# Kernel optimization log

Measured on AMD Instinct MI355X. Metric: run time of the kernel, lower is better.

The kernel has to match this reference:

```python
import jax, jax.numpy as jnp
import numpy as np


def _wasserstein_1d(xs, a, b, p):
    # POT-style 1D OT loss on shared sorted support xs: sum over merged
    # quantile levels of |F_a^{-1}(q) - F_b^{-1}(q)|^p * dq  (no p-th root).
    n = xs.shape[0]
    cdf_a = jnp.cumsum(a)
    cdf_b = jnp.cumsum(b)
    qs = jnp.sort(jnp.concatenate([cdf_a, cdf_b]))  # [2n] merged quantile levels
    qa = xs[jnp.clip(jnp.searchsorted(cdf_a, qs), 0, n - 1)]
    qb = xs[jnp.clip(jnp.searchsorted(cdf_b, qs), 0, n - 1)]
    qs_pad = jnp.concatenate([jnp.zeros((1,), qs.dtype), qs])
    delta = qs_pad[1:] - qs_pad[:-1]
    return jnp.sum(delta * jnp.abs(qa - qb) ** p)


def setup_inputs() -> dict:
    key = jax.random.key(0)
    k1, k2 = jax.random.split(key)
    N = 8388608      # samples
    NBINS = 10       # discretization
    G = 4            # number of groups
    acts = jax.random.normal(k1, (N,), dtype=jnp.float32)
    group_labels = jax.random.randint(k2, (N,), 0, G, dtype=jnp.int32)
    bary_est = jnp.ones((NBINS,), jnp.float32) / NBINS  # learned barycenter param, init 1/n
    return {"acts": acts, "bary_est": bary_est, "group_labels": group_labels,
            "nbins": NBINS, "n_groups": G}


def reference(acts, bary_est, group_labels, nbins, n_groups):
    r = 1.0 / nbins
    locs = jnp.arange(0, 1, r, dtype=acts.dtype)              # [nbins] bin centers
    c = jax.nn.sigmoid(acts) - 0.0001                         # [N] cdf-mapped samples
    # triangular-kernel soft histogram contributions: [N, nbins]
    K = jax.nn.relu(r - jnp.abs(c[:, None] - locs[None, :]))
    # per-group bin counts (torch.unique returns sorted labels 0..G-1)
    counts = jax.ops.segment_sum(K, group_labels, num_segments=n_groups)  # [G, nbins]
    h = counts + 0.0001
    h = h / jnp.sum(h, axis=1, keepdims=True)   # HistoBin norm
    h = h / jnp.sum(h, axis=1, keepdims=True)   # genHists renorm (mathematical no-op, kept for fidelity)
    xs = jnp.arange(nbins, dtype=acts.dtype)    # POT support bins 0..n-1
    losses = jax.vmap(lambda hg: _wasserstein_1d(xs, hg, bary_est, 2))(h)  # [G]
    loss = jnp.sum(losses).reshape(1)
    return loss, bary_est
```

## Files before the change

kernel.cpp:

```cpp
#include <hip/hip_runtime.h>

#define NBINS 10
#define NG 4
#define NH (NG * NBINS)
#define TPB 128
#define NBLOCKS 2048
#define PACKF 32.0f

__device__ __forceinline__ void proc1(float x, int g, float* col) {
    float ex = __expf(-x);
    float rc = __builtin_amdgcn_rcpf(1.0f + ex);
    float p  = __builtin_fmaf(rc, 10.0f, -0.001f);
    float fj = floorf(p);
    float u  = p - fj;
    int j0 = max((int)fj, 0);
    int row = g * NBINS + j0;
    col[row * TPB] += (PACKF + u);
}

__device__ __forceinline__ void proc4(float4 a, int4 g, float* col) {
    proc1(a.x, g.x, col); proc1(a.y, g.y, col);
    proc1(a.z, g.z, col); proc1(a.w, g.w, col);
}

__global__ void __launch_bounds__(TPB) wb_hist(const float4* __restrict__ acts,
                                               const int4* __restrict__ labels,
                                               const float* __restrict__ acts_s,
                                               const int* __restrict__ labels_s,
                                               float* __restrict__ parts,
                                               int n4, int n, int nparts) {
    __shared__ float lh[NH * TPB];
    const int tid = threadIdx.x;
    #pragma unroll
    for (int i = 0; i < NH; ++i) lh[i * TPB + tid] = 0.0f;
    __syncthreads();

    float* col = &lh[tid];
    const int gsz = gridDim.x * TPB;
    int idx = blockIdx.x * TPB + tid;
    for (; idx + 3 * gsz < n4; idx += 4 * gsz) {
        float4 a0 = acts[idx];
        float4 a1 = acts[idx + gsz];
        float4 a2 = acts[idx + 2 * gsz];
        float4 a3 = acts[idx + 3 * gsz];
        int4 g0 = labels[idx];
        int4 g1 = labels[idx + gsz];
        int4 g2 = labels[idx + 2 * gsz];
        int4 g3 = labels[idx + 3 * gsz];
        proc4(a0, g0, col); proc4(a1, g1, col);
        proc4(a2, g2, col); proc4(a3, g3, col);
    }
    for (; idx < n4; idx += gsz) proc4(acts[idx], labels[idx], col);

    if (blockIdx.x == 0 && tid == 0) {
        for (int i = n4 * 4; i < n; ++i) proc1(acts_s[i], labels_s[i], col);
    }
    __syncthreads();

    if (tid < NH) {
        float n_sum = 0.0f, u_sum = 0.0f;
        for (int k = 0; k < TPB; ++k) {
            float acc = lh[tid * TPB + ((tid + k) & (TPB - 1))];
            float nc = floorf(acc * (1.0f / PACKF));
            n_sum += nc;
            u_sum += acc - PACKF * nc;
        }
        float u_prev = __shfl_up(u_sum, 1);
        if ((tid % NBINS) == 0) u_prev = 0.0f;
        parts[tid * nparts + blockIdx.x] = 0.1f * (n_sum - u_sum + u_prev);
    }
}

__global__ void __launch_bounds__(1024) wb_final(const float4* __restrict__ parts4,
                                                 const float* __restrict__ bary,
                                                 float* __restrict__ out, int nparts) {
    __shared__ float hist[NH];
    __shared__ float bsh[NBINS];
    __shared__ float losses[NG];

    if (threadIdx.x < NBINS) {
        float b = bary[threadIdx.x];
        bsh[threadIdx.x] = b;
        out[1 + threadIdx.x] = b;
    }

    const int q4 = nparts >> 2;
    int wave = threadIdx.x >> 6, lane = threadIdx.x & 63;
    for (int j = wave; j < NH; j += 16) {
        float s = 0.0f;
        for (int i = lane; i < q4; i += 64) {
            float4 v = parts4[j * q4 + i];
            s += (v.x + v.y) + (v.z + v.w);
        }
        #pragma unroll
        for (int off = 32; off; off >>= 1) s += __shfl_down(s, off);
        if (lane == 0) hist[j] = s;
    }
    __syncthreads();

    if (threadIdx.x < NG) {
        const int gI = threadIdx.x;
        float h[NBINS];
        float s = 0.0f;
        #pragma unroll
        for (int j = 0; j < NBINS; ++j) { h[j] = hist[gI * NBINS + j] + 0.0001f; s += h[j]; }
        #pragma unroll
        for (int j = 0; j < NBINS; ++j) h[j] /= s;
        float s2 = 0.0f;
        #pragma unroll
        for (int j = 0; j < NBINS; ++j) s2 += h[j];
        #pragma unroll
        for (int j = 0; j < NBINS; ++j) h[j] /= s2;

        float cdfa[NBINS], cdfb[NBINS];
        float acc = 0.0f;
        #pragma unroll
        for (int j = 0; j < NBINS; ++j) { acc += h[j]; cdfa[j] = acc; }
        acc = 0.0f;
        #pragma unroll
        for (int j = 0; j < NBINS; ++j) { acc += bsh[j]; cdfb[j] = acc; }
        float T = fmaxf(cdfa[NBINS - 1], cdfb[NBINS - 1]);
        cdfa[NBINS - 1] = T;
        cdfb[NBINS - 1] = T;

        float loss = 0.0f, lo_a = 0.0f;
        #pragma unroll
        for (int i = 0; i < NBINS; ++i) {
            float hi_a = cdfa[i];
            float lo_b = 0.0f;
            #pragma unroll
            for (int j = 0; j < NBINS; ++j) {
                float hi_b = cdfb[j];
                float ov = fminf(hi_a, hi_b) - fmaxf(lo_a, lo_b);
                float w = (float)((i - j) * (i - j));
                loss += fmaxf(ov, 0.0f) * w;
                lo_b = hi_b;
            }
            lo_a = hi_a;
        }
        losses[gI] = loss;
    }
    __syncthreads();
    if (threadIdx.x == 0)
        out[0] = losses[0] + losses[1] + losses[2] + losses[3];
}

extern "C" void kernel_launch(void* const* d_in, const int* in_sizes, int n_in,
                              void* d_out, int out_size, void* d_ws, size_t ws_size,
                              hipStream_t stream) {
    const float* acts   = (const float*)d_in[0];
    const float* bary   = (const float*)d_in[1];
    const int*   labels = (const int*)d_in[2];
    float* outp  = (float*)d_out;
    float* parts = (float*)d_ws;
    int N  = in_sizes[0];
    int n4 = N >> 2;

    wb_hist<<<NBLOCKS, TPB, 0, stream>>>((const float4*)acts, (const int4*)labels,
                                         acts, labels, parts, n4, N, NBLOCKS);
    wb_final<<<1, 1024, 0, stream>>>((const float4*)parts, bary, outp, NBLOCKS);
}
```

Baseline: 31.56 us.

## Fuse histogram and final loss kernels with last-block ticket reduction

```diff
diff --git a/kernel.cpp b/kernel.cpp
--- a/kernel.cpp
+++ b/kernel.cpp
@@ -23,13 +23,20 @@
     proc1(a.z, g.z, col); proc1(a.w, g.w, col);
 }
 
-__global__ void __launch_bounds__(TPB) wb_hist(const float4* __restrict__ acts,
-                                               const int4* __restrict__ labels,
-                                               const float* __restrict__ acts_s,
-                                               const int* __restrict__ labels_s,
-                                               float* __restrict__ parts,
-                                               int n4, int n, int nparts) {
+__global__ void __launch_bounds__(TPB) wb_fused(const float4* __restrict__ acts,
+                                                const int4* __restrict__ labels,
+                                                const float* __restrict__ acts_s,
+                                                const int* __restrict__ labels_s,
+                                                const float* __restrict__ bary,
+                                                float* __restrict__ out,
+                                                float* __restrict__ parts,
+                                                unsigned int* __restrict__ ticket,
+                                                int n4, int n) {
     __shared__ float lh[NH * TPB];
+    float* hist   = &lh[0];
+    float* losses = &lh[48];
+    volatile unsigned int* lastflag = (volatile unsigned int*)&lh[56];
+
     const int tid = threadIdx.x;
     #pragma unroll
     for (int i = 0; i < NH; ++i) lh[i * TPB + tid] = 0.0f;
@@ -67,39 +74,39 @@
         }
         float u_prev = __shfl_up(u_sum, 1);
         if ((tid % NBINS) == 0) u_prev = 0.0f;
-        parts[tid * nparts + blockIdx.x] = 0.1f * (n_sum - u_sum + u_prev);
-    }
-}
-
-__global__ void __launch_bounds__(1024) wb_final(const float4* __restrict__ parts4,
-                                                 const float* __restrict__ bary,
-                                                 float* __restrict__ out, int nparts) {
-    __shared__ float hist[NH];
-    __shared__ float bsh[NBINS];
-    __shared__ float losses[NG];
-
-    if (threadIdx.x < NBINS) {
-        float b = bary[threadIdx.x];
-        bsh[threadIdx.x] = b;
-        out[1 + threadIdx.x] = b;
-    }
-
-    const int q4 = nparts >> 2;
-    int wave = threadIdx.x >> 6, lane = threadIdx.x & 63;
-    for (int j = wave; j < NH; j += 16) {
-        float s = 0.0f;
-        for (int i = lane; i < q4; i += 64) {
-            float4 v = parts4[j * q4 + i];
-            s += (v.x + v.y) + (v.z + v.w);
-        }
-        #pragma unroll
-        for (int off = 32; off; off >>= 1) s += __shfl_down(s, off);
-        if (lane == 0) hist[j] = s;
+        float hb = 0.1f * (n_sum - u_sum + u_prev);
+        __hip_atomic_store(&parts[tid * NBLOCKS + blockIdx.x], hb,
+                           __ATOMIC_RELAXED, __HIP_MEMORY_SCOPE_AGENT);
     }
     __syncthreads();
 
-    if (threadIdx.x < NG) {
-        const int gI = threadIdx.x;
+    if (tid == 0) {
+        unsigned int old = __hip_atomic_fetch_add(ticket, 1u, __ATOMIC_RELAXED,
+                                                  __HIP_MEMORY_SCOPE_AGENT);
+        *lastflag = (old == (unsigned int)(NBLOCKS - 1)) ? 1u : 0u;
+    }
+    __syncthreads();
+    if (*lastflag == 0u) return;
+
+    {
+        int wave = tid >> 6, lane = tid & 63;
+        for (int j = wave; j < NH; j += 2) {
+            float s = 0.0f;
+            #pragma unroll
+            for (int k = 0; k < NBLOCKS / 64; ++k)
+                s += __hip_atomic_load(&parts[j * NBLOCKS + lane + k * 64],
+                                       __ATOMIC_RELAXED, __HIP_MEMORY_SCOPE_AGENT);
+            #pragma unroll
+            for (int off = 32; off; off >>= 1) s += __shfl_down(s, off);
+            if (lane == 0) hist[j] = s;
+        }
+    }
+    if (tid >= NH && tid < NH + NBINS)
+        out[1 + (tid - NH)] = bary[tid - NH];
+    __syncthreads();
+
+    if (tid < NG) {
+        const int gI = tid;
         float h[NBINS];
         float s = 0.0f;
         #pragma unroll
@@ -118,7 +125,7 @@
         for (int j = 0; j < NBINS; ++j) { acc += h[j]; cdfa[j] = acc; }
         acc = 0.0f;
         #pragma unroll
-        for (int j = 0; j < NBINS; ++j) { acc += bsh[j]; cdfb[j] = acc; }
+        for (int j = 0; j < NBINS; ++j) { acc += bary[j]; cdfb[j] = acc; }
         float T = fmaxf(cdfa[NBINS - 1], cdfb[NBINS - 1]);
         cdfa[NBINS - 1] = T;
         cdfb[NBINS - 1] = T;
@@ -141,7 +148,7 @@
         losses[gI] = loss;
     }
     __syncthreads();
-    if (threadIdx.x == 0)
+    if (tid == 0)
         out[0] = losses[0] + losses[1] + losses[2] + losses[3];
 }
 
@@ -151,12 +158,14 @@
     const float* acts   = (const float*)d_in[0];
     const float* bary   = (const float*)d_in[1];
     const int*   labels = (const int*)d_in[2];
-    float* outp  = (float*)d_out;
-    float* parts = (float*)d_ws;
+    float* outp = (float*)d_out;
+    unsigned int* ticket = (unsigned int*)d_ws;
+    float* parts = (float*)((char*)d_ws + 256);
     int N  = in_sizes[0];
     int n4 = N >> 2;
 
-    wb_hist<<<NBLOCKS, TPB, 0, stream>>>((const float4*)acts, (const int4*)labels,
-                                         acts, labels, parts, n4, N, NBLOCKS);
-    wb_final<<<1, 1024, 0, stream>>>((const float4*)parts, bary, outp, NBLOCKS);
+    hipMemsetAsync(ticket, 0, sizeof(unsigned int), stream);
+    wb_fused<<<NBLOCKS, TPB, 0, stream>>>((const float4*)acts, (const int4*)labels,
+                                          acts, labels, bary, outp,
+                                          parts, ticket, n4, N);
 }
```

Result: slower. 58.19 us (+84.4%).

## Pack histogram bins as quantized 16-bit halves and double block size

Applied to the files above, without the earlier changes.

```diff
diff --git a/kernel.cpp b/kernel.cpp
--- a/kernel.cpp
+++ b/kernel.cpp
@@ -3,22 +3,25 @@
 #define NBINS 10
 #define NG 4
 #define NH (NG * NBINS)
-#define TPB 128
+#define TPB 256
 #define NBLOCKS 2048
-#define PACKF 32.0f
+#define NROWS2 (NH / 2)
+#define INVUQ (1.0f / 63.0f)
 
-__device__ __forceinline__ void proc1(float x, int g, float* col) {
+__device__ __forceinline__ void proc1(float x, int g, unsigned int* col) {
     float ex = __expf(-x);
     float rc = __builtin_amdgcn_rcpf(1.0f + ex);
     float p  = __builtin_fmaf(rc, 10.0f, -0.001f);
     float fj = floorf(p);
     float u  = p - fj;
+    int uq = (int)__builtin_fmaf(u, 63.0f, 0.5f);
     int j0 = max((int)fj, 0);
     int row = g * NBINS + j0;
-    col[row * TPB] += (PACKF + u);
+    unsigned int val = (2048u + (unsigned)uq) << ((row & 1) << 4);
+    col[(row >> 1) * TPB] += val;
 }
 
-__device__ __forceinline__ void proc4(float4 a, int4 g, float* col) {
+__device__ __forceinline__ void proc4(float4 a, int4 g, unsigned int* col) {
     proc1(a.x, g.x, col); proc1(a.y, g.y, col);
     proc1(a.z, g.z, col); proc1(a.w, g.w, col);
 }
@@ -29,13 +32,13 @@
                                                const int* __restrict__ labels_s,
                                                float* __restrict__ parts,
                                                int n4, int n, int nparts) {
-    __shared__ float lh[NH * TPB];
+    __shared__ unsigned int lh[NROWS2 * TPB];
     const int tid = threadIdx.x;
     #pragma unroll
-    for (int i = 0; i < NH; ++i) lh[i * TPB + tid] = 0.0f;
+    for (int i = 0; i < NROWS2; ++i) lh[i * TPB + tid] = 0u;
     __syncthreads();
 
-    float* col = &lh[tid];
+    unsigned int* col = &lh[tid];
     const int gsz = gridDim.x * TPB;
     int idx = blockIdx.x * TPB + tid;
     for (; idx + 3 * gsz < n4; idx += 4 * gsz) {
@@ -57,17 +60,34 @@
     }
     __syncthreads();
 
+    unsigned int nA = 0, sA = 0;
+    if (tid < 160) {
+        int row = tid % NH, chunk = tid / NH;
+        int sh = (row & 1) << 4;
+        const unsigned int* base = &lh[(row >> 1) * TPB + chunk * 64];
+        #pragma unroll
+        for (int k = 0; k < 64; ++k) {
+            unsigned int f = (base[(row + k) & 63] >> sh) & 0xFFFFu;
+            nA += f >> 11;
+            sA += f & 0x7FFu;
+        }
+    }
+    __syncthreads();
+    if (tid < 160) lh[tid] = (nA << 16) | sA;
+    __syncthreads();
+
     if (tid < NH) {
-        float n_sum = 0.0f, u_sum = 0.0f;
-        for (int k = 0; k < TPB; ++k) {
-            float acc = lh[tid * TPB + ((tid + k) & (TPB - 1))];
-            float nc = floorf(acc * (1.0f / PACKF));
-            n_sum += nc;
-            u_sum += acc - PACKF * nc;
+        unsigned int n_sum = 0, s_sum = 0;
+        #pragma unroll
+        for (int c = 0; c < 4; ++c) {
+            unsigned int f = lh[c * NH + tid];
+            n_sum += f >> 16;
+            s_sum += f & 0xFFFFu;
         }
+        float u_sum = (float)s_sum * INVUQ;
         float u_prev = __shfl_up(u_sum, 1);
         if ((tid % NBINS) == 0) u_prev = 0.0f;
-        parts[tid * nparts + blockIdx.x] = 0.1f * (n_sum - u_sum + u_prev);
+        parts[tid * nparts + blockIdx.x] = 0.1f * ((float)n_sum - u_sum + u_prev);
     }
 }
 
```

Result: slower. 32.46 us (+2.9%).
